# Optimization experiments

Measured on AMD Instinct MI355X. Metric: run time of the kernel, lower is better.

The kernel has to match this reference:

```python
import jax, jax.numpy as jnp
import numpy as np

B, S, E = 4, 2048, 1024
H, D = 16, 64  # num_heads, attention_head_dim


def setup_inputs() -> dict:
    key = jax.random.key(0)
    ks = jax.random.split(key, 9)
    scale_e = 1.0 / np.sqrt(E)
    scale_hd = 1.0 / np.sqrt(H * D)
    x = jax.random.normal(ks[0], (B, S, E), dtype=jnp.float32)
    # per-head projection weights, stacked: [H, E, D]
    Wq = jax.random.uniform(ks[1], (H, E, D), minval=-scale_e, maxval=scale_e, dtype=jnp.float32)
    Wk = jax.random.uniform(ks[2], (H, E, D), minval=-scale_e, maxval=scale_e, dtype=jnp.float32)
    Wv = jax.random.uniform(ks[3], (H, E, D), minval=-scale_e, maxval=scale_e, dtype=jnp.float32)
    bq = jax.random.uniform(ks[4], (H, D), minval=-scale_e, maxval=scale_e, dtype=jnp.float32)
    bk = jax.random.uniform(ks[5], (H, D), minval=-scale_e, maxval=scale_e, dtype=jnp.float32)
    bv = jax.random.uniform(ks[6], (H, D), minval=-scale_e, maxval=scale_e, dtype=jnp.float32)
    Wo = jax.random.uniform(ks[7], (H * D, E), minval=-scale_hd, maxval=scale_hd, dtype=jnp.float32)
    bo = jax.random.uniform(ks[8], (E,), minval=-scale_hd, maxval=scale_hd, dtype=jnp.float32)
    return {"x": x, "Wq": Wq, "Wk": Wk, "Wv": Wv, "bq": bq, "bk": bk, "bv": bv, "Wo": Wo, "bo": bo}


def reference(x, Wq, Wk, Wv, bq, bk, bv, Wo, bo):
    # Per-head QKV projections, vectorized over heads: [B,H,S,D]
    Q = jnp.einsum('bse,hed->bhsd', x, Wq) + bq[None, :, None, :]
    K = jnp.einsum('bse,hed->bhsd', x, Wk) + bk[None, :, None, :]
    V = jnp.einsum('bse,hed->bhsd', x, Wv) + bv[None, :, None, :]
    scale = 1.0 / jnp.sqrt(jnp.asarray(D, dtype=Q.dtype))
    scores = jnp.einsum('bhsd,bhtd->bhst', Q, K) * scale  # [B,H,S,S]
    attn = jax.nn.softmax(scores, axis=-1)
    Z = jnp.einsum('bhst,bhtd->bhsd', attn, V)            # [B,H,S,D]
    # concat heads on feature dim -> [B,S,H*D], then output projection
    Zc = jnp.transpose(Z, (0, 2, 1, 3)).reshape(B, S, H * D)
    return Zc @ Wo + bo
```

## Files before the change

### kernel.cpp

```cpp
#include <hip/hip_runtime.h>


typedef __attribute__((ext_vector_type(4)))  float   f32x4;
typedef __attribute__((ext_vector_type(16))) float   f32x16;
typedef __attribute__((ext_vector_type(8)))  __bf16  bf16x8;
typedef __attribute__((ext_vector_type(4)))  __bf16  bf16x4;
typedef __attribute__((ext_vector_type(4)))  unsigned int u32x4;
typedef unsigned int u32;

#if __has_builtin(__builtin_amdgcn_exp2f)
#define EXP2F(x) __builtin_amdgcn_exp2f(x)
#else
#define EXP2F(x) exp2f(x)
#endif

__device__ __forceinline__ f32x4 fzero4() {
    f32x4 z = {0.f, 0.f, 0.f, 0.f};
    return z;
}
__device__ __forceinline__ f32x16 fzero16() {
    f32x16 z;
#pragma unroll
    for (int i = 0; i < 16; i++) z[i] = 0.f;
    return z;
}

__device__ __forceinline__ u32 cvtpk_bf16(float lo, float hi_) {
    u32 r;
    asm("v_cvt_pk_bf16_f32 %0, %1, %2" : "=v"(r) : "v"(lo), "v"(hi_));
    return r;
}

__device__ __forceinline__ void gload_lds16(const void* g, void* l) {
    __builtin_amdgcn_global_load_lds(
        (const __attribute__((address_space(1))) u32*)g,
        (__attribute__((address_space(3))) u32*)l, 16, 0, 0);
}

__global__ __launch_bounds__(256) void cvt_f32_bf16_4(
    const float* __restrict__ s, __bf16* __restrict__ d, long n) {
    long i = ((long)blockIdx.x * 256 + threadIdx.x) * 4;
    if (i >= n) return;
    float4 v = *(const float4*)(s + i);
    bf16x4 o = { (__bf16)v.x, (__bf16)v.y, (__bf16)v.z, (__bf16)v.w };
    *(bf16x4*)(d + i) = o;
}

__global__ __launch_bounds__(256) void pack_w_t(
    const float* __restrict__ src, __bf16* __restrict__ dst, int R, int C) {
    __shared__ float t[32][33];
    const int z = blockIdx.z;
    src += (size_t)z * R * C;
    dst += (size_t)z * R * C;
    const int r0 = blockIdx.x * 32, c0 = blockIdx.y * 32;
    const int x = threadIdx.x, y = threadIdx.y;
#pragma unroll
    for (int i = 0; i < 4; i++)
        t[y + i * 8][x] = src[(size_t)(r0 + y + i * 8) * C + c0 + x];
    __syncthreads();
#pragma unroll
    for (int i = 0; i < 4; i++)
        dst[(size_t)(c0 + y + i * 8) * R + r0 + x] = (__bf16)t[x][y + i * 8];
}

__global__ __launch_bounds__(256) void pack_bias(
    const float* __restrict__ bq, const float* __restrict__ bk,
    const float* __restrict__ bv, float* __restrict__ bqkv) {
    int n = blockIdx.x * 256 + threadIdx.x;
    if (n >= 3072) return;
    int t = n >> 10, r = n & 1023;
    const float* s = (t == 0) ? bq : (t == 1) ? bk : bv;
    bqkv[n] = s[r];
}

#define GEMM_STAGE(BUF, KOFF)                                                  \
  {                                                                            \
    gload_lds16(A + arow0 * K + (KOFF) + kcol,                                 \
                (char*)As + (BUF) * 16384 + wid * 1024);                       \
    gload_lds16(A + arow1 * K + (KOFF) + kcol,                                 \
                (char*)As + (BUF) * 16384 + 8192 + wid * 1024);                \
    gload_lds16(Bt + brow * K + (KOFF) + kcol,                                 \
                (char*)Bs + (BUF) * 8192 + wid * 1024);                        \
  }

#define GEMM_COMPUTE(BUF)                                                      \
  {                                                                            \
    bf16x8 a[4], b[4];                                                         \
    _Pragma("unroll")                                                          \
    for (int mi = 0; mi < 4; mi++)                                             \
      a[mi] = *(const bf16x8*)&As[(BUF) * 8192 +                               \
                                  (mr * 64 + mi * 16 + l15) * 32 + l4 * 8];    \
    _Pragma("unroll")                                                          \
    for (int ni = 0; ni < 4; ni++)                                             \
      b[ni] = *(const bf16x8*)&Bs[(BUF) * 4096 +                               \
                                  (nc * 64 + ni * 16 + l15) * 32 + l4 * 8];    \
    _Pragma("unroll")                                                          \
    for (int mi = 0; mi < 4; mi++)                                             \
      _Pragma("unroll")                                                        \
      for (int ni = 0; ni < 4; ni++)                                           \
        acc[mi][ni] = __builtin_amdgcn_mfma_f32_16x16x32_bf16(                 \
            a[mi], b[ni], acc[mi][ni], 0, 0, 0);                               \
  }

#define GEMM_PREAMBLE                                                          \
    const int tid  = threadIdx.x;                                              \
    const int lane = tid & 63, wid = tid >> 6;                                 \
    const int mr = wid >> 1, nc = wid & 1;                                     \
    const int l15 = lane & 15, l4 = lane >> 4;                                 \
    const int bn = blockIdx.x, bm = blockIdx.y;                                \
    const long arow0 = (long)bm * 256 + (tid >> 2);                            \
    const long arow1 = arow0 + 128;                                            \
    const long brow  = (long)bn * 128 + (tid >> 2);                            \
    const int  kcol  = (tid & 3) * 8;                                          \
    f32x4 acc[4][4];                                                           \
    _Pragma("unroll")                                                          \
    for (int i = 0; i < 4; i++)                                                \
      _Pragma("unroll")                                                        \
      for (int j = 0; j < 4; j++) acc[i][j] = fzero4();                        \
    GEMM_STAGE(0, 0)                                                           \
    __syncthreads();                                                           \
    int cur = 0;                                                               \
    for (int k0 = 0; k0 < K; k0 += 32, cur ^= 1) {                             \
        if (k0 + 32 < K) GEMM_STAGE(cur ^ 1, k0 + 32)                          \
        GEMM_COMPUTE(cur)                                                      \
        __syncthreads();                                                       \
    }

template <bool F32OUT>
__global__ __launch_bounds__(512) void gemm_bt(
    const __bf16* __restrict__ A, const __bf16* __restrict__ Bt,
    const float* __restrict__ bias, void* __restrict__ Cout,
    int M, int N, int K, int ldc) {
    __shared__ __bf16 As[2 * 256 * 32];
    __shared__ __bf16 Bs[2 * 128 * 32];
    GEMM_PREAMBLE

#pragma unroll
    for (int mi = 0; mi < 4; mi++)
#pragma unroll
        for (int ni = 0; ni < 4; ni++) {
            const int row = bm * 256 + mr * 64 + mi * 16 + l4 * 4;
            const int col = bn * 128 + nc * 64 + ni * 16 + l15;
            const float bv = bias ? bias[col] : 0.f;
#pragma unroll
            for (int r = 0; r < 4; r++) {
                float v = acc[mi][ni][r] + bv;
                if (F32OUT)
                    ((float*)Cout)[(long)(row + r) * ldc + col] = v;
                else
                    ((__bf16*)Cout)[(long)(row + r) * ldc + col] = (__bf16)v;
            }
        }
}

__global__ __launch_bounds__(512) void gemm_qkv(
    const __bf16* __restrict__ A, const __bf16* __restrict__ Bt,
    const float* __restrict__ bias, __bf16* __restrict__ QKV,
    __bf16* __restrict__ VT, int K) {
    __shared__ __bf16 As[2 * 256 * 32];
    __shared__ __bf16 Bs[2 * 128 * 32];
    GEMM_PREAMBLE

    if (bn < 16) {
#pragma unroll
        for (int mi = 0; mi < 4; mi++)
#pragma unroll
            for (int ni = 0; ni < 4; ni++) {
                const int row = bm * 256 + mr * 64 + mi * 16 + l4 * 4;
                const int col = bn * 128 + nc * 64 + ni * 16 + l15;
                const float bv = bias[col];
#pragma unroll
                for (int r = 0; r < 4; r++)
                    QKV[(long)(row + r) * 3072 + col] =
                        (__bf16)(acc[mi][ni][r] + bv);
            }
    } else {
#pragma unroll
        for (int mi = 0; mi < 4; mi++)
#pragma unroll
            for (int ni = 0; ni < 4; ni++) {
                const int row = bm * 256 + mr * 64 + mi * 16 + l4 * 4;
                const int col = bn * 128 + nc * 64 + ni * 16 + l15;
                const float bv = bias[col];
                const int vcol = col - 2048;
                const int h = vcol >> 6, dcol = vcol & 63;
                const int bb = row >> 11, s = row & 2047;
                bf16x4 o;
#pragma unroll
                for (int r = 0; r < 4; r++)
                    o[r] = (__bf16)(acc[mi][ni][r] + bv);
                *(bf16x4*)&VT[((size_t)(bb * 16 + h) * 64 + dcol) * 2048 + s] = o;
            }
    }
}

__global__ __launch_bounds__(256, 4) void attn_fwd(
    const __bf16* __restrict__ QKV, const __bf16* __restrict__ VT,
    __bf16* __restrict__ Z) {
    const int S = 2048, LDQ = 3072;
    const int dd = blockIdx.x;
    const int blk = (dd & 7) * 128 + (dd >> 3);
    const int qt = blk & 15, bh = blk >> 4, b = bh >> 4, h = bh & 15;
    const int tid = threadIdx.x, wid = tid >> 6, lane = tid & 63;
    const int l31 = lane & 31, hi = lane >> 5;

    __shared__ __bf16 smem[16384];

    const __bf16* Qb = QKV + (size_t)b * S * LDQ + h * 64;
    const __bf16* Kb = Qb + 1024;
    const __bf16* Vb = VT + (size_t)bh * 64 * S;
    const int qrow = qt * 128 + wid * 32;

    bf16x8 qf[4];
#pragma unroll
    for (int kk = 0; kk < 4; kk++)
        qf[kk] = *(const bf16x8*)(Qb + (size_t)(qrow + l31) * LDQ + kk * 16 + hi * 8);

    const int f0 = wid * 2, f1 = wid * 2 + 1;
    const int kr0 = (f0 >> 2) * 32 + l31, kc0 = (f0 & 3) * 16 + hi * 8;
    const int kr1 = (f1 >> 2) * 32 + l31, kc1 = (f1 & 3) * 16 + hi * 8;
    const int vr0 = kr0, vs0 = kc0;
    const int vr1 = kr1, vs1 = kc1;
    const int ldst = lane * 16;

    f32x16 o0 = fzero16(), o1 = fzero16();
    float m_r = -1e30f, l_r = 0.f;
    const float csc = 0.18033688011f;

    gload_lds16(Kb + (size_t)kr0 * LDQ + kc0, (char*)smem + f0 * 1024 + ldst);
    gload_lds16(Kb + (size_t)kr1 * LDQ + kc1, (char*)smem + f1 * 1024 + ldst);
    gload_lds16(Vb + (size_t)vr0 * S + vs0,   (char*)smem + 16384 + f0 * 1024 + ldst);
    gload_lds16(Vb + (size_t)vr1 * S + vs1,   (char*)smem + 16384 + f1 * 1024 + ldst);
    asm volatile("s_waitcnt vmcnt(0)" ::: "memory");
    __syncthreads();

    int cur = 0;
    for (int t0 = 0; t0 < S; t0 += 64, cur ^= 1) {
        if (t0 + 64 < S) {
            char* kl = (char*)smem + (cur ^ 1) * 8192;
            char* vl = (char*)smem + 16384 + (cur ^ 1) * 8192;
            gload_lds16(Kb + (size_t)(t0 + 64 + kr0) * LDQ + kc0, kl + f0 * 1024 + ldst);
            gload_lds16(Kb + (size_t)(t0 + 64 + kr1) * LDQ + kc1, kl + f1 * 1024 + ldst);
            gload_lds16(Vb + (size_t)vr0 * S + t0 + 64 + vs0,     vl + f0 * 1024 + ldst);
            gload_lds16(Vb + (size_t)vr1 * S + t0 + 64 + vs1,     vl + f1 * 1024 + ldst);
        }
        const char* kbase = (const char*)smem + cur * 8192;
        const char* vbase = (const char*)smem + 16384 + cur * 8192;

        bf16x8 kf[8];
#pragma unroll
        for (int f = 0; f < 8; f++)
            kf[f] = *(const bf16x8*)(kbase + f * 1024 + ldst);
        f32x16 s0 = fzero16(), s1 = fzero16();
        __builtin_amdgcn_s_setprio(1);
#pragma unroll
        for (int kk = 0; kk < 4; kk++) {
            s0 = __builtin_amdgcn_mfma_f32_32x32x16_bf16(kf[kk],     qf[kk], s0, 0, 0, 0);
            s1 = __builtin_amdgcn_mfma_f32_32x32x16_bf16(kf[4 + kk], qf[kk], s1, 0, 0, 0);
        }
        __builtin_amdgcn_s_setprio(0);

        float mm[16];
#pragma unroll
        for (int i = 0; i < 16; i++) mm[i] = fmaxf(s0[i], s1[i]);
#pragma unroll
        for (int st = 8; st >= 1; st >>= 1)
#pragma unroll
            for (int i = 0; i < st; i++) mm[i] = fmaxf(mm[i], mm[i + st]);
        const float pm = fmaxf(mm[0], __shfl_xor(mm[0], 32));
        if (!__all(pm - m_r <= 64.f)) {
            const float mnew = fmaxf(m_r, pm);
            const float alpha = EXP2F((m_r - mnew) * csc);
            m_r = mnew;
            l_r *= alpha;
#pragma unroll
            for (int i = 0; i < 16; i++) { o0[i] *= alpha; o1[i] *= alpha; }
        }
        const float mc = m_r * csc;
        float ss[16];
#pragma unroll
        for (int i = 0; i < 16; i++) {
            float p0 = EXP2F(s0[i] * csc - mc); s0[i] = p0;
            float p1 = EXP2F(s1[i] * csc - mc); s1[i] = p1;
            ss[i] = p0 + p1;
        }
#pragma unroll
        for (int st = 8; st >= 1; st >>= 1)
#pragma unroll
            for (int i = 0; i < st; i++) ss[i] += ss[i + st];
        l_r += ss[0] + __shfl_xor(ss[0], 32);

        __builtin_amdgcn_s_setprio(1);
#pragma unroll
        for (int kkt = 0; kkt < 4; kkt++) {
            const int r0 = (kkt & 1) * 8;
            u32 w0, w1, w2, w3;
            if (kkt < 2) {
                w0 = cvtpk_bf16(s0[r0],     s0[r0 + 1]);
                w1 = cvtpk_bf16(s0[r0 + 2], s0[r0 + 3]);
                w2 = cvtpk_bf16(s0[r0 + 4], s0[r0 + 5]);
                w3 = cvtpk_bf16(s0[r0 + 6], s0[r0 + 7]);
            } else {
                w0 = cvtpk_bf16(s1[r0],     s1[r0 + 1]);
                w1 = cvtpk_bf16(s1[r0 + 2], s1[r0 + 3]);
                w2 = cvtpk_bf16(s1[r0 + 4], s1[r0 + 5]);
                w3 = cvtpk_bf16(s1[r0 + 6], s1[r0 + 7]);
            }
            asm("v_permlane32_swap_b32 %0, %1" : "+v"(w0), "+v"(w2));
            asm("v_permlane32_swap_b32 %0, %1" : "+v"(w1), "+v"(w3));
            u32x4 pw = {w0, w1, w2, w3};
            bf16x8 pf = __builtin_bit_cast(bf16x8, pw);
            bf16x8 vf0 = *(const bf16x8*)(vbase + kkt * 1024 + ldst);
            bf16x8 vf1 = *(const bf16x8*)(vbase + (4 + kkt) * 1024 + ldst);
            o0 = __builtin_amdgcn_mfma_f32_32x32x16_bf16(vf0, pf, o0, 0, 0, 0);
            o1 = __builtin_amdgcn_mfma_f32_32x32x16_bf16(vf1, pf, o1, 0, 0, 0);
        }
        __builtin_amdgcn_s_setprio(0);

        asm volatile("s_waitcnt vmcnt(0)" ::: "memory");
        __syncthreads();
    }

    const float inv = 1.0f / l_r;
    __bf16 (*Tl)[72] = (__bf16 (*)[72])smem;
    const int trow = wid * 32 + l31;
#pragma unroll
    for (int g = 0; g < 4; g++) {
        bf16x4 t4a, t4b;
#pragma unroll
        for (int j = 0; j < 4; j++) {
            t4a[j] = (__bf16)(o0[4 * g + j] * inv);
            t4b[j] = (__bf16)(o1[4 * g + j] * inv);
        }
        *(bf16x4*)&Tl[trow][g * 8 + hi * 4]      = t4a;
        *(bf16x4*)&Tl[trow][32 + g * 8 + hi * 4] = t4b;
    }
    asm volatile("s_waitcnt lgkmcnt(0)" ::: "memory");
    __builtin_amdgcn_sched_barrier(0);

    const int rr = wid * 32 + (lane >> 1);
    const int ch = (lane & 1) * 32;
#pragma unroll
    for (int i = 0; i < 4; i++) {
        bf16x8 z = *(const bf16x8*)&Tl[rr][ch + i * 8];
        *(bf16x8*)&Z[((size_t)b * S + qt * 128 + rr) * 1024 + h * 64 + ch + i * 8] = z;
    }
}

extern "C" void kernel_launch(void* const* d_in, const int* in_sizes, int n_in,
                              void* d_out, int out_size, void* d_ws, size_t ws_size,
                              hipStream_t stream) {
    const float* x  = (const float*)d_in[0];
    const float* Wq = (const float*)d_in[1];
    const float* Wk = (const float*)d_in[2];
    const float* Wv = (const float*)d_in[3];
    const float* bq = (const float*)d_in[4];
    const float* bk = (const float*)d_in[5];
    const float* bv = (const float*)d_in[6];
    const float* Wo = (const float*)d_in[7];
    const float* bo = (const float*)d_in[8];
    float* out = (float*)d_out;

    char* p = (char*)d_ws;
    __bf16* xb   = (__bf16*)p; p += 8192L * 1024 * 2;
    __bf16* Wqkv = (__bf16*)p; p += 3072L * 1024 * 2;
    float*  bqkv = (float*)p;  p += 3072L * 4;
    __bf16* QKV  = (__bf16*)p; p += 8192L * 3072 * 2;
    __bf16* VTb  = (__bf16*)p; p += 64L * 64 * 2048 * 2;
    __bf16* Zb   = (__bf16*)p; p += 8192L * 1024 * 2;
    __bf16* Wot  = (__bf16*)p; p += 1024L * 1024 * 2;

    cvt_f32_bf16_4<<<8192, 256, 0, stream>>>(x, xb, 8192L * 1024);
    pack_w_t<<<dim3(32, 2, 16), dim3(32, 8), 0, stream>>>(Wq, Wqkv,                1024, 64);
    pack_w_t<<<dim3(32, 2, 16), dim3(32, 8), 0, stream>>>(Wk, Wqkv + 1024L * 1024, 1024, 64);
    pack_w_t<<<dim3(32, 2, 16), dim3(32, 8), 0, stream>>>(Wv, Wqkv + 2048L * 1024, 1024, 64);
    pack_w_t<<<dim3(32, 32, 1), dim3(32, 8), 0, stream>>>(Wo, Wot, 1024, 1024);
    pack_bias<<<12, 256, 0, stream>>>(bq, bk, bv, bqkv);

    gemm_qkv<<<dim3(24, 32), 512, 0, stream>>>(xb, Wqkv, bqkv, QKV, VTb, 1024);
    attn_fwd<<<1024, 256, 0, stream>>>(QKV, VTb, Zb);
    gemm_bt<true><<<dim3(8, 32), 512, 0, stream>>>(Zb, Wot, bo, out,
                                                   8192, 1024, 1024, 1024);
}
```

Before: 226.3 us.

## Merge prep kernels into one launch and compute softmax row sums via MFMA

Folds the six preprocessing launches (x conversion, three QKV weight transposes, Wo transpose, bias pack) into one kernel that dispatches on block index, cutting per-launch overhead. In attention, the per-row softmax denominator is now taken from an extra MFMA against a vector of ones, using the bf16-rounded probabilities, instead of a VALU reduction tree plus a cross-lane shuffle. This takes VALU work off the softmax path but adds a third MFMA per V step and sums rounded rather than fp32 probabilities, which slightly changes the normalisation.

```diff
diff --git a/kernel.cpp b/kernel.cpp
--- a/kernel.cpp
+++ b/kernel.cpp
@@ -37,40 +37,61 @@
         (__attribute__((address_space(3))) u32*)l, 16, 0, 0);
 }
 
-__global__ __launch_bounds__(256) void cvt_f32_bf16_4(
-    const float* __restrict__ s, __bf16* __restrict__ d, long n) {
-    long i = ((long)blockIdx.x * 256 + threadIdx.x) * 4;
-    if (i >= n) return;
-    float4 v = *(const float4*)(s + i);
-    bf16x4 o = { (__bf16)v.x, (__bf16)v.y, (__bf16)v.z, (__bf16)v.w };
-    *(bf16x4*)(d + i) = o;
-}
-
-__global__ __launch_bounds__(256) void pack_w_t(
-    const float* __restrict__ src, __bf16* __restrict__ dst, int R, int C) {
-    __shared__ float t[32][33];
-    const int z = blockIdx.z;
-    src += (size_t)z * R * C;
-    dst += (size_t)z * R * C;
-    const int r0 = blockIdx.x * 32, c0 = blockIdx.y * 32;
-    const int x = threadIdx.x, y = threadIdx.y;
-#pragma unroll
-    for (int i = 0; i < 4; i++)
-        t[y + i * 8][x] = src[(size_t)(r0 + y + i * 8) * C + c0 + x];
-    __syncthreads();
-#pragma unroll
-    for (int i = 0; i < 4; i++)
-        dst[(size_t)(c0 + y + i * 8) * R + r0 + x] = (__bf16)t[x][y + i * 8];
-}
-
-__global__ __launch_bounds__(256) void pack_bias(
+__global__ __launch_bounds__(256) void prep(
+    const float* __restrict__ x,  __bf16* __restrict__ xb,
+    const float* __restrict__ Wq, const float* __restrict__ Wk,
+    const float* __restrict__ Wv, const float* __restrict__ Wo,
+    __bf16* __restrict__ Wqkv, __bf16* __restrict__ Wot,
     const float* __restrict__ bq, const float* __restrict__ bk,
     const float* __restrict__ bv, float* __restrict__ bqkv) {
-    int n = blockIdx.x * 256 + threadIdx.x;
-    if (n >= 3072) return;
-    int t = n >> 10, r = n & 1023;
-    const float* s = (t == 0) ? bq : (t == 1) ? bk : bv;
-    bqkv[n] = s[r];
+    __shared__ float t[32][33];
+    const int tid = threadIdx.x;
+    int bid = blockIdx.x;
+
+    if (bid < 8192) {
+        long i = ((long)bid * 256 + tid) * 4;
+        float4 v = *(const float4*)(x + i);
+        bf16x4 o = { (__bf16)v.x, (__bf16)v.y, (__bf16)v.z, (__bf16)v.w };
+        *(bf16x4*)(xb + i) = o;
+        return;
+    }
+    bid -= 8192;
+    if (bid < 4096) {
+        const float* src;
+        __bf16* dst;
+        int C, r0, c0;
+        if (bid < 3072) {
+            const int g = bid >> 10, rem = bid & 1023;
+            const float* W = (g == 0) ? Wq : (g == 1) ? Wk : Wv;
+            const int z = rem >> 6, bx = rem & 31, by = (rem >> 5) & 1;
+            C = 64;
+            src = W + (size_t)z * 1024 * 64;
+            dst = Wqkv + (size_t)g * 1024 * 1024 + (size_t)z * 1024 * 64;
+            r0 = bx * 32; c0 = by * 32;
+        } else {
+            const int rem = bid - 3072;
+            const int bx = rem & 31, by = rem >> 5;
+            C = 1024;
+            src = Wo; dst = Wot;
+            r0 = bx * 32; c0 = by * 32;
+        }
+        const int xx = tid & 31, yy = tid >> 5;
+#pragma unroll
+        for (int i = 0; i < 4; i++)
+            t[yy + i * 8][xx] = src[(size_t)(r0 + yy + i * 8) * C + c0 + xx];
+        __syncthreads();
+#pragma unroll
+        for (int i = 0; i < 4; i++)
+            dst[(size_t)(c0 + yy + i * 8) * 1024 + r0 + xx] =
+                (__bf16)t[xx][yy + i * 8];
+        return;
+    }
+    const int n = (bid - 4096) * 256 + tid;
+    if (n < 3072) {
+        const int tt = n >> 10, r = n & 1023;
+        const float* s = (tt == 0) ? bq : (tt == 1) ? bk : bv;
+        bqkv[n] = s[r];
+    }
 }
 
 #define GEMM_STAGE(BUF, KOFF)                                                  \
@@ -223,9 +244,11 @@
     const int vr1 = kr1, vs1 = kc1;
     const int ldst = lane * 16;
 
-    f32x16 o0 = fzero16(), o1 = fzero16();
-    float m_r = -1e30f, l_r = 0.f;
+    f32x16 o0 = fzero16(), o1 = fzero16(), l_acc = fzero16();
+    float m_r = -1e30f;
     const float csc = 0.18033688011f;
+    const __bf16 onebf = (__bf16)1.0f;
+    const bf16x8 ones8 = {onebf, onebf, onebf, onebf, onebf, onebf, onebf, onebf};
 
     gload_lds16(Kb + (size_t)kr0 * LDQ + kc0, (char*)smem + f0 * 1024 + ldst);
     gload_lds16(Kb + (size_t)kr1 * LDQ + kc1, (char*)smem + f1 * 1024 + ldst);
@@ -272,23 +295,16 @@
             const float mnew = fmaxf(m_r, pm);
             const float alpha = EXP2F((m_r - mnew) * csc);
             m_r = mnew;
-            l_r *= alpha;
+            l_acc[0] *= alpha;
 #pragma unroll
             for (int i = 0; i < 16; i++) { o0[i] *= alpha; o1[i] *= alpha; }
         }
         const float mc = m_r * csc;
-        float ss[16];
 #pragma unroll
         for (int i = 0; i < 16; i++) {
-            float p0 = EXP2F(s0[i] * csc - mc); s0[i] = p0;
-            float p1 = EXP2F(s1[i] * csc - mc); s1[i] = p1;
-            ss[i] = p0 + p1;
-        }
-#pragma unroll
-        for (int st = 8; st >= 1; st >>= 1)
-#pragma unroll
-            for (int i = 0; i < st; i++) ss[i] += ss[i + st];
-        l_r += ss[0] + __shfl_xor(ss[0], 32);
+            s0[i] = EXP2F(s0[i] * csc - mc);
+            s1[i] = EXP2F(s1[i] * csc - mc);
+        }
 
         __builtin_amdgcn_s_setprio(1);
 #pragma unroll
@@ -314,6 +330,7 @@
             bf16x8 vf1 = *(const bf16x8*)(vbase + (4 + kkt) * 1024 + ldst);
             o0 = __builtin_amdgcn_mfma_f32_32x32x16_bf16(vf0, pf, o0, 0, 0, 0);
             o1 = __builtin_amdgcn_mfma_f32_32x32x16_bf16(vf1, pf, o1, 0, 0, 0);
+            l_acc = __builtin_amdgcn_mfma_f32_32x32x16_bf16(ones8, pf, l_acc, 0, 0, 0);
         }
         __builtin_amdgcn_s_setprio(0);
 
@@ -321,7 +338,7 @@
         __syncthreads();
     }
 
-    const float inv = 1.0f / l_r;
+    const float inv = 1.0f / l_acc[0];
     __bf16 (*Tl)[72] = (__bf16 (*)[72])smem;
     const int trow = wid * 32 + l31;
 #pragma unroll
@@ -370,12 +387,8 @@
     __bf16* Zb   = (__bf16*)p; p += 8192L * 1024 * 2;
     __bf16* Wot  = (__bf16*)p; p += 1024L * 1024 * 2;
 
-    cvt_f32_bf16_4<<<8192, 256, 0, stream>>>(x, xb, 8192L * 1024);
-    pack_w_t<<<dim3(32, 2, 16), dim3(32, 8), 0, stream>>>(Wq, Wqkv,                1024, 64);
-    pack_w_t<<<dim3(32, 2, 16), dim3(32, 8), 0, stream>>>(Wk, Wqkv + 1024L * 1024, 1024, 64);
-    pack_w_t<<<dim3(32, 2, 16), dim3(32, 8), 0, stream>>>(Wv, Wqkv + 2048L * 1024, 1024, 64);
-    pack_w_t<<<dim3(32, 32, 1), dim3(32, 8), 0, stream>>>(Wo, Wot, 1024, 1024);
-    pack_bias<<<12, 256, 0, stream>>>(bq, bk, bv, bqkv);
+    prep<<<12300, 256, 0, stream>>>(x, xb, Wq, Wk, Wv, Wo, Wqkv, Wot,
+                                    bq, bk, bv, bqkv);
 
     gemm_qkv<<<dim3(24, 32), 512, 0, stream>>>(xb, Wqkv, bqkv, QKV, VTb, 1024);
     attn_fwd<<<1024, 256, 0, stream>>>(QKV, VTb, Zb);
```

After: 244.4 us. 1.08x slower.
